# Kernel optimization log

Measured on AMD Instinct MI355X. Metric: run time of the kernel, lower is better.

The kernel has to match this reference:

```python
import jax, jax.numpy as jnp
import numpy as np
import math

ETA = 1.0          # self.ddim_sampling_eta
SCALE = 1.0        # self.scale (unused in eval ddim path here)
IOU_THR = 0.5
SCORE_THR = 0.5


def cosine_alphas_cumprod(timesteps=1000, s=0.008):
    steps = timesteps + 1
    x = np.linspace(0, timesteps, steps, dtype=np.float64)
    ac = np.cos((x / timesteps + s) / (1 + s) * math.pi * 0.5) ** 2
    ac = ac / ac[0]
    betas = np.clip(1 - ac[1:] / ac[:-1], 0, 0.999)
    alphas = 1.0 - betas
    return np.cumprod(alphas).astype(np.float32)  # [timesteps]


def setup_inputs() -> dict:
    key = jax.random.key(0)
    ks = jax.random.split(key, 8)
    B, N, C, H = 128, 500, 80, 6
    boxes_t = jax.random.normal(ks[0], (B, N, 2), dtype=jnp.float32)
    predicted_class = jax.random.normal(ks[1], (H, B, N, C), dtype=jnp.float32)
    predicted_boxes = jax.random.uniform(ks[2], (H, B, N, 2), dtype=jnp.float32)
    noise = jax.random.normal(ks[3], (B, N, 2), dtype=jnp.float32)
    fresh_noise = jax.random.normal(ks[4], (B, N, 2), dtype=jnp.float32)
    alphas_cumprod = jnp.asarray(cosine_alphas_cumprod(1000))
    return {
        "boxes_t": boxes_t,
        "predicted_class": predicted_class,
        "predicted_boxes": predicted_boxes,
        "noise": noise,
        "fresh_noise": fresh_noise,
        "alphas_cumprod": alphas_cumprod,
        "t_now": 999,
        "t_next": 499,
    }


def _nms_1d_single(boxes_cw, scores, labels):
    # boxes_cw: [N,2] (center, width) 1-D intervals; class-aware greedy NMS.
    N = boxes_cw.shape[0]
    c = boxes_cw[:, 0]
    w = jnp.maximum(boxes_cw[:, 1], 1e-4)
    x1, x2 = c - w / 2, c + w / 2
    inter = jnp.maximum(0.0, jnp.minimum(x2[:, None], x2[None, :])
                        - jnp.maximum(x1[:, None], x1[None, :]))
    union = w[:, None] + w[None, :] - inter
    iou = inter / jnp.maximum(union, 1e-9)                       # [N,N]
    same = labels[:, None] == labels[None, :]
    order = jnp.argsort(-scores)
    iou_s = iou[order][:, order]
    same_s = same[order][:, order]
    idx = jnp.arange(N)

    def body(i, suppressed):
        keep_i = jnp.logical_not(suppressed[i])
        row = keep_i & (iou_s[i] > IOU_THR) & same_s[i] & (idx > i)
        return suppressed | row

    suppressed = jax.lax.fori_loop(0, N, body, jnp.zeros((N,), bool))
    keep_sorted = jnp.logical_not(suppressed)
    return jnp.zeros((N,), bool).at[order].set(keep_sorted)      # original order


def reference(boxes_t, predicted_class, predicted_boxes, noise, fresh_noise,
              alphas_cumprod, t_now, t_next):
    ac = alphas_cumprod
    boxes_start = predicted_boxes[-1]                            # [B,N,2]

    # predict_noise_from_start (extract -> scalar gather at t_now)
    sqrt_recip = jnp.sqrt(1.0 / ac[t_now])
    sqrt_recipm1 = jnp.sqrt(1.0 / ac[t_now] - 1.0)
    pred_noise = (sqrt_recip * boxes_t - boxes_start) / sqrt_recipm1

    # box renewal: keep mask from sigmoid-max of predicted_class[-1][0]
    score0 = jax.nn.sigmoid(predicted_class[-1][0])              # [N,C]
    keep = jnp.max(score0, axis=-1) > SCORE_THR                  # [N]

    # DDIM step
    alpha, alpha_next = ac[t_now], ac[t_next]
    sigma = ETA * jnp.sqrt((1 - alpha / alpha_next) * (1 - alpha_next) / (1 - alpha))
    cc = jnp.sqrt(1 - alpha_next - sigma ** 2)
    upd = boxes_start * jnp.sqrt(alpha_next) + cc * pred_noise + sigma * noise
    # removed slots are renewed with fresh gaussian proposals (mask form of concat)
    boxes_next = jnp.where(keep[None, :, None], upd, fresh_noise)  # [B,N,2]

    # postprocessing: softmax over classes (drop last bg class), max -> scores/labels
    probs = jax.nn.softmax(predicted_class[-1], axis=-1)[:, :, :-1]  # [B,N,C-1]
    scores = jnp.max(probs, axis=-1)                             # [B,N]
    labels = jnp.argmax(probs, axis=-1)                          # [B,N]
    nms_keep = jax.vmap(_nms_1d_single)(boxes_start, scores, labels)  # [B,N] bool

    return boxes_next, scores, labels, nms_keep
```

## Files before the change

### kernel.cpp

```cpp
#include <hip/hip_runtime.h>
#include <float.h>

#define BB 128
#define NN 500
#define CC 80
#define NH 6
#define NP 512

typedef unsigned long long u64;
typedef unsigned int u32;

__global__ __launch_bounds__(256) void scores_labels_keep_kernel(
    const float* __restrict__ pc,
    float* __restrict__ scores,
    float* __restrict__ labels,
    int* __restrict__ keep) {
    const int rl = threadIdx.x >> 2;
    const int q = threadIdx.x & 3;
    const int row = blockIdx.x * 64 + rl;
    if (row >= BB * NN) return;

    const float4* base = (const float4*)(pc + (size_t)(NH - 1) * BB * NN * CC);
    float4 v[5];
#pragma unroll
    for (int k = 0; k < 5; ++k) v[k] = base[(size_t)row * 20 + q + 4 * k];

    float m = v[0].x;
#pragma unroll
    for (int k = 0; k < 5; ++k) {
        m = fmaxf(m, v[k].x); m = fmaxf(m, v[k].y);
        m = fmaxf(m, v[k].z); m = fmaxf(m, v[k].w);
    }
    m = fmaxf(m, __shfl_xor(m, 1));
    m = fmaxf(m, __shfl_xor(m, 2));

    float s = 0.0f;
#pragma unroll
    for (int k = 0; k < 5; ++k) {
        s += expf(v[k].x - m); s += expf(v[k].y - m);
        s += expf(v[k].z - m); s += expf(v[k].w - m);
    }
    s += __shfl_xor(s, 1);
    s += __shfl_xor(s, 2);

    float bv = -FLT_MAX; int bc = 1000;
#pragma unroll
    for (int k = 0; k < 5; ++k) {
        const float* vf = (const float*)&v[k];
#pragma unroll
        for (int j = 0; j < 4; ++j) {
            int c = (q + 4 * k) * 4 + j;
            float val = vf[j];
            if (c < CC - 1 && (val > bv || (val == bv && c < bc))) { bv = val; bc = c; }
        }
    }
#pragma unroll
    for (int off = 1; off < 4; off <<= 1) {
        float ov = __shfl_xor(bv, off);
        int oc = __shfl_xor(bc, off);
        if (ov > bv || (ov == bv && oc < bc)) { bv = ov; bc = oc; }
    }

    if (q == 0) {
        scores[row] = expf(bv - m) / s;
        labels[row] = (float)bc;
        if (row < NN) keep[row] = (m > 0.0f) ? 1 : 0;
    }
}

__global__ void boxes_next_kernel(const float* __restrict__ boxes_t,
                                  const float* __restrict__ pb,
                                  const float* __restrict__ noise,
                                  const float* __restrict__ fresh,
                                  const float* __restrict__ ac,
                                  const int* __restrict__ t_now_p,
                                  const int* __restrict__ t_next_p,
                                  const int* __restrict__ keep,
                                  float* __restrict__ out) {
    int i = blockIdx.x * blockDim.x + threadIdx.x;
    if (i >= BB * NN) return;
    int n = i % NN;
    int tn = t_now_p[0], tx = t_next_p[0];
    float a = ac[tn], an = ac[tx];
    float sqrt_recip = sqrtf(1.0f / a);
    float sqrt_recipm1 = sqrtf(1.0f / a - 1.0f);
    float sigma = sqrtf((1.0f - a / an) * (1.0f - an) / (1.0f - a));
    float cc = sqrtf(1.0f - an - sigma * sigma);
    float sqan = sqrtf(an);
    const float2 bt = ((const float2*)boxes_t)[i];
    const float2 bs = ((const float2*)(pb + (size_t)(NH - 1) * BB * NN * 2))[i];
    float2 o;
    if (keep[n]) {
        const float2 nz = ((const float2*)noise)[i];
        float pn0 = (sqrt_recip * bt.x - bs.x) / sqrt_recipm1;
        float pn1 = (sqrt_recip * bt.y - bs.y) / sqrt_recipm1;
        o.x = bs.x * sqan + cc * pn0 + sigma * nz.x;
        o.y = bs.y * sqan + cc * pn1 + sigma * nz.y;
    } else {
        o = ((const float2*)fresh)[i];
    }
    ((float2*)out)[i] = o;
}

__global__ __launch_bounds__(512) void nms_kernel(const float* __restrict__ pb,
                                                  const float* __restrict__ scores,
                                                  const float* __restrict__ labels,
                                                  float* __restrict__ keep_out) {
    __shared__ float4 scs4[NP / 4];
    __shared__ float4 box4u[NP];
    __shared__ float4 sbox4[NP];
    __shared__ int order[NP];
    __shared__ unsigned char lab8[NP];
    __shared__ short brank_s[NP];
    __shared__ short member[NP];
    __shared__ int hist[CC];
    __shared__ int boff[CC];
    __shared__ unsigned char supp[NP];

    const int b = blockIdx.x;
    const int tid = threadIdx.x;
    float* scs = (float*)scs4;

    const float2* boxes = (const float2*)(pb + (size_t)(NH - 1) * BB * NN * 2) + (size_t)b * NN;
    const float* sc = scores + (size_t)b * NN;
    const float* lb = labels + (size_t)b * NN;

    if (tid < CC) hist[tid] = 0;
    if (tid < NN) {
        float2 cw = boxes[tid];
        float w = fmaxf(cw.y, 0.0001f);
        box4u[tid] = make_float4(cw.x - w * 0.5f, cw.x + w * 0.5f, w,
                                 __int_as_float((int)lb[tid]));
        scs[tid] = sc[tid];
    } else {
        box4u[tid] = make_float4(0.f, 0.f, 0.f, __int_as_float(255));
        scs[tid] = -FLT_MAX;
    }
    supp[tid] = 0;
    __syncthreads();

    {
        float si = scs[tid];
        int r = 0;
        for (int j4 = 0; j4 < NP / 4; ++j4) {
            float4 s4 = scs4[j4];
            int j = j4 * 4;
            r += (s4.x > si) || (s4.x == si && (j + 0) < tid);
            r += (s4.y > si) || (s4.y == si && (j + 1) < tid);
            r += (s4.z > si) || (s4.z == si && (j + 2) < tid);
            r += (s4.w > si) || (s4.w == si && (j + 3) < tid);
        }
        order[r] = tid;
    }
    __syncthreads();

    {
        float4 v = box4u[order[tid]];
        sbox4[tid] = v;
        lab8[tid] = (unsigned char)__float_as_int(v.w);
    }
    __syncthreads();

    if (tid < NN) {
        const u32 myl = lab8[tid];
        int cnt = 0;
        const uint4* l16 = (const uint4*)lab8;
        const int nc = (tid >> 4) + 1;
        for (int cI = 0; cI < nc; ++cI) {
            uint4 c = l16[cI];
            int base = cI * 16;
#pragma unroll
            for (int byi = 0; byi < 4; ++byi) {
                cnt += (base + byi      < tid) && (((c.x >> (8 * byi)) & 0xFF) == myl);
                cnt += (base + 4 + byi  < tid) && (((c.y >> (8 * byi)) & 0xFF) == myl);
                cnt += (base + 8 + byi  < tid) && (((c.z >> (8 * byi)) & 0xFF) == myl);
                cnt += (base + 12 + byi < tid) && (((c.w >> (8 * byi)) & 0xFF) == myl);
            }
        }
        brank_s[tid] = (short)cnt;
        atomicAdd(&hist[myl], 1);
    }
    __syncthreads();
    if (tid == 0) {
        int s = 0;
        for (int l = 0; l < CC; ++l) { boff[l] = s; s += hist[l]; }
    }
    __syncthreads();
    if (tid < NN) member[boff[lab8[tid]] + brank_s[tid]] = (short)tid;
    __syncthreads();

    {
        const int lane = tid & 63;
        const int wv = tid >> 6;
        const int l = lane * 8 + wv;
        if (l < CC) {
            const int n = hist[l], off = boff[l];
            for (int p = 0; p < n - 1; ++p) {
                const int rp = member[off + p];
                if (supp[rp]) continue;
                const float4 bp = sbox4[rp];
                for (int q = p + 1; q < n; ++q) {
                    const int rq = member[off + q];
                    if (supp[rq]) continue;
                    const float4 bq = sbox4[rq];
                    float inter = fminf(bp.y, bq.y) - fmaxf(bp.x, bq.x);
                    if (inter > 0.0f) {
                        float uni = bp.z + bq.z - inter;
                        float iou = inter / fmaxf(uni, 1e-9f);
                        if (iou > 0.5f) supp[rq] = 1;
                    }
                }
            }
        }
    }
    __syncthreads();

    if (tid < NN) {
        keep_out[(size_t)b * NN + order[tid]] = supp[tid] ? 0.0f : 1.0f;
    }
}

extern "C" void kernel_launch(void* const* d_in, const int* in_sizes, int n_in,
                              void* d_out, int out_size, void* d_ws, size_t ws_size,
                              hipStream_t stream) {
    const float* boxes_t = (const float*)d_in[0];
    const float* pc      = (const float*)d_in[1];
    const float* pb      = (const float*)d_in[2];
    const float* noise   = (const float*)d_in[3];
    const float* fresh   = (const float*)d_in[4];
    const float* ac      = (const float*)d_in[5];
    const int*   t_now   = (const int*)d_in[6];
    const int*   t_next  = (const int*)d_in[7];

    float* out_boxes  = (float*)d_out;
    float* out_scores = out_boxes + (size_t)BB * NN * 2;
    float* out_labels = out_scores + (size_t)BB * NN;
    float* out_keep   = out_labels + (size_t)BB * NN;

    int* keep_ws = (int*)d_ws;

    scores_labels_keep_kernel<<<(BB * NN) / 64, 256, 0, stream>>>(
        pc, out_scores, out_labels, keep_ws);
    boxes_next_kernel<<<(BB * NN + 255) / 256, 256, 0, stream>>>(
        boxes_t, pb, noise, fresh, ac, t_now, t_next, keep_ws, out_boxes);
    nms_kernel<<<BB, 512, 0, stream>>>(pb, out_scores, out_labels, out_keep);
}
```

Measured before the change: 221.9 us.

## Fuse DDIM box update into NMS kernel and parallelize per-class NMS across wave lanes

Removes the separate boxes_next kernel and computes the DDIM update inside the NMS kernel's load phase, reusing the already loaded predicted boxes. The serial per-class prefix sum becomes a wave-level shuffle scan. Per-class greedy NMS now maps one class to a whole wavefront, with lanes holding candidates and ballot/readlane broadcasting each pivot, replacing one thread per class walking an O(n^2) loop. Classes with more than 64 members fall back to a single-lane serial loop.

```diff
diff --git a/kernel.cpp b/kernel.cpp
--- a/kernel.cpp
+++ b/kernel.cpp
@@ -68,43 +68,17 @@
     }
 }
 
-__global__ void boxes_next_kernel(const float* __restrict__ boxes_t,
-                                  const float* __restrict__ pb,
-                                  const float* __restrict__ noise,
-                                  const float* __restrict__ fresh,
-                                  const float* __restrict__ ac,
-                                  const int* __restrict__ t_now_p,
-                                  const int* __restrict__ t_next_p,
-                                  const int* __restrict__ keep,
-                                  float* __restrict__ out) {
-    int i = blockIdx.x * blockDim.x + threadIdx.x;
-    if (i >= BB * NN) return;
-    int n = i % NN;
-    int tn = t_now_p[0], tx = t_next_p[0];
-    float a = ac[tn], an = ac[tx];
-    float sqrt_recip = sqrtf(1.0f / a);
-    float sqrt_recipm1 = sqrtf(1.0f / a - 1.0f);
-    float sigma = sqrtf((1.0f - a / an) * (1.0f - an) / (1.0f - a));
-    float cc = sqrtf(1.0f - an - sigma * sigma);
-    float sqan = sqrtf(an);
-    const float2 bt = ((const float2*)boxes_t)[i];
-    const float2 bs = ((const float2*)(pb + (size_t)(NH - 1) * BB * NN * 2))[i];
-    float2 o;
-    if (keep[n]) {
-        const float2 nz = ((const float2*)noise)[i];
-        float pn0 = (sqrt_recip * bt.x - bs.x) / sqrt_recipm1;
-        float pn1 = (sqrt_recip * bt.y - bs.y) / sqrt_recipm1;
-        o.x = bs.x * sqan + cc * pn0 + sigma * nz.x;
-        o.y = bs.y * sqan + cc * pn1 + sigma * nz.y;
-    } else {
-        o = ((const float2*)fresh)[i];
-    }
-    ((float2*)out)[i] = o;
-}
-
 __global__ __launch_bounds__(512) void nms_kernel(const float* __restrict__ pb,
                                                   const float* __restrict__ scores,
                                                   const float* __restrict__ labels,
+                                                  const float* __restrict__ boxes_t,
+                                                  const float* __restrict__ noise,
+                                                  const float* __restrict__ fresh,
+                                                  const float* __restrict__ ac,
+                                                  const int* __restrict__ t_now_p,
+                                                  const int* __restrict__ t_next_p,
+                                                  const int* __restrict__ keep_ws,
+                                                  float* __restrict__ out_boxes,
                                                   float* __restrict__ keep_out) {
     __shared__ float4 scs4[NP / 4];
     __shared__ float4 box4u[NP];
@@ -126,17 +100,40 @@
     const float* lb = labels + (size_t)b * NN;
 
     if (tid < CC) hist[tid] = 0;
+    supp[tid] = 0;
     if (tid < NN) {
         float2 cw = boxes[tid];
         float w = fmaxf(cw.y, 0.0001f);
         box4u[tid] = make_float4(cw.x - w * 0.5f, cw.x + w * 0.5f, w,
                                  __int_as_float((int)lb[tid]));
         scs[tid] = sc[tid];
+
+        {
+            const size_t i = (size_t)b * NN + tid;
+            int tn = t_now_p[0], tx = t_next_p[0];
+            float a = ac[tn], an = ac[tx];
+            float sqrt_recip = sqrtf(1.0f / a);
+            float sqrt_recipm1 = sqrtf(1.0f / a - 1.0f);
+            float sigma = sqrtf((1.0f - a / an) * (1.0f - an) / (1.0f - a));
+            float ccf = sqrtf(1.0f - an - sigma * sigma);
+            float sqan = sqrtf(an);
+            const float2 bt = ((const float2*)boxes_t)[i];
+            float2 o;
+            if (keep_ws[tid]) {
+                const float2 nz = ((const float2*)noise)[i];
+                float pn0 = (sqrt_recip * bt.x - cw.x) / sqrt_recipm1;
+                float pn1 = (sqrt_recip * bt.y - cw.y) / sqrt_recipm1;
+                o.x = cw.x * sqan + ccf * pn0 + sigma * nz.x;
+                o.y = cw.y * sqan + ccf * pn1 + sigma * nz.y;
+            } else {
+                o = ((const float2*)fresh)[i];
+            }
+            ((float2*)out_boxes)[i] = o;
+        }
     } else {
         box4u[tid] = make_float4(0.f, 0.f, 0.f, __int_as_float(255));
         scs[tid] = -FLT_MAX;
     }
-    supp[tid] = 0;
     __syncthreads();
 
     {
@@ -181,33 +178,75 @@
         atomicAdd(&hist[myl], 1);
     }
     __syncthreads();
-    if (tid == 0) {
-        int s = 0;
-        for (int l = 0; l < CC; ++l) { boff[l] = s; s += hist[l]; }
-    }
-    __syncthreads();
+
+    if (tid < 64) {
+        int a = (tid < CC) ? hist[tid] : 0;
+        int b2 = (tid < CC - 64) ? hist[64 + tid] : 0;
+        int sa = a;
+#pragma unroll
+        for (int d = 1; d < 64; d <<= 1) {
+            int t = __shfl_up(sa, d);
+            if ((int)tid >= d) sa += t;
+        }
+        int totalA = __shfl(sa, 63);
+        int sb = b2;
+#pragma unroll
+        for (int d = 1; d < 64; d <<= 1) {
+            int t = __shfl_up(sb, d);
+            if ((int)tid >= d) sb += t;
+        }
+        if (tid < CC) boff[tid] = sa - a;
+        if (tid < CC - 64) boff[64 + tid] = sb - b2 + totalA;
+    }
+    __syncthreads();
+
     if (tid < NN) member[boff[lab8[tid]] + brank_s[tid]] = (short)tid;
     __syncthreads();
 
     {
+        const int wv = tid >> 6;
         const int lane = tid & 63;
-        const int wv = tid >> 6;
-        const int l = lane * 8 + wv;
-        if (l < CC) {
-            const int n = hist[l], off = boff[l];
-            for (int p = 0; p < n - 1; ++p) {
-                const int rp = member[off + p];
-                if (supp[rp]) continue;
-                const float4 bp = sbox4[rp];
-                for (int q = p + 1; q < n; ++q) {
-                    const int rq = member[off + q];
-                    if (supp[rq]) continue;
-                    const float4 bq = sbox4[rq];
-                    float inter = fminf(bp.y, bq.y) - fmaxf(bp.x, bq.x);
-                    if (inter > 0.0f) {
-                        float uni = bp.z + bq.z - inter;
-                        float iou = inter / fmaxf(uni, 1e-9f);
-                        if (iou > 0.5f) supp[rq] = 1;
+        for (int l = wv; l < CC; l += 8) {
+            const int n = hist[l];
+            if (n <= 1) continue;
+            const int off = boff[l];
+            if (n <= 64) {
+                const bool valid = lane < n;
+                int rq = 0;
+                float x1 = 0.f, x2 = 0.f, ww = 0.f;
+                if (valid) {
+                    rq = member[off + lane];
+                    float4 v = sbox4[rq];
+                    x1 = v.x; x2 = v.y; ww = v.z;
+                }
+                bool sup = false;
+                for (int p = 0; p < n - 1; ++p) {
+                    u64 smask = __ballot(sup);
+                    bool pAlive = ((smask >> p) & 1ull) == 0ull;
+                    float bx1 = __int_as_float(__builtin_amdgcn_readlane(__float_as_int(x1), p));
+                    float bx2 = __int_as_float(__builtin_amdgcn_readlane(__float_as_int(x2), p));
+                    float bw  = __int_as_float(__builtin_amdgcn_readlane(__float_as_int(ww), p));
+                    float inter = fmaxf(0.0f, fminf(bx2, x2) - fmaxf(bx1, x1));
+                    float uni = bw + ww - inter;
+                    float iou = inter / fmaxf(uni, 1e-9f);
+                    sup = sup || (pAlive && valid && (lane > p) && (iou > 0.5f));
+                }
+                if (valid && sup) supp[rq] = 1;
+            } else {
+                if (lane == 0) {
+                    for (int p = 0; p < n - 1; ++p) {
+                        int rp = member[off + p];
+                        if (supp[rp]) continue;
+                        float4 bp = sbox4[rp];
+                        for (int q2 = p + 1; q2 < n; ++q2) {
+                            int rqq = member[off + q2];
+                            if (supp[rqq]) continue;
+                            float4 bq = sbox4[rqq];
+                            float inter = fmaxf(0.0f, fminf(bp.y, bq.y) - fmaxf(bp.x, bq.x));
+                            float uni = bp.z + bq.z - inter;
+                            float iou = inter / fmaxf(uni, 1e-9f);
+                            if (iou > 0.5f) supp[rqq] = 1;
+                        }
                     }
                 }
             }
@@ -241,7 +280,7 @@
 
     scores_labels_keep_kernel<<<(BB * NN) / 64, 256, 0, stream>>>(
         pc, out_scores, out_labels, keep_ws);
-    boxes_next_kernel<<<(BB * NN + 255) / 256, 256, 0, stream>>>(
-        boxes_t, pb, noise, fresh, ac, t_now, t_next, keep_ws, out_boxes);
-    nms_kernel<<<BB, 512, 0, stream>>>(pb, out_scores, out_labels, out_keep);
+    nms_kernel<<<BB, 512, 0, stream>>>(pb, out_scores, out_labels,
+                                       boxes_t, noise, fresh, ac, t_now, t_next,
+                                       keep_ws, out_boxes, out_keep);
 }
```

After: 214.7 us. 3.2% less time.
